# Optimization experiments

Hardware: AMD Instinct MI355X
Metric: run time of the kernel (lower is better)

## Reference

```python
import jax, jax.numpy as jnp
import numpy as np

B, T = 4096, 512
H_ENC, H_DEC = 4, 10


def _cell(x_t, h, c, Wih, Whh, b):
    # PyTorch LSTM cell, gate order i, f, g, o
    g = x_t @ Wih.T + h @ Whh.T + b
    i, f, gg, o = jnp.split(g, 4, axis=-1)
    c = jax.nn.sigmoid(f) * c + jax.nn.sigmoid(i) * jnp.tanh(gg)
    h = jax.nn.sigmoid(o) * jnp.tanh(c)
    return h, c


def _lstm_layer(x_seq, Wih, Whh, bih, bhh):
    # x_seq: [B, T, in] -> outputs [B, T, H], final (h, c) [B, H]
    b = bih + bhh
    Bn = x_seq.shape[0]
    H = Whh.shape[1]
    init = (jnp.zeros((Bn, H), x_seq.dtype), jnp.zeros((Bn, H), x_seq.dtype))

    def step(carry, xt):
        h, c = carry
        h, c = _cell(xt, h, c, Wih, Whh, b)
        return (h, c), h

    (hT, cT), ys = jax.lax.scan(step, init, jnp.swapaxes(x_seq, 0, 1))
    return jnp.swapaxes(ys, 0, 1), hT, cT


def setup_inputs() -> dict:
    key = jax.random.key(0)
    ks = iter(jax.random.split(key, 32))
    p = lambda *s: jax.random.normal(next(ks), s, dtype=jnp.float32) * 0.1
    return {
        "x": jax.random.normal(next(ks), (B, T, 1), dtype=jnp.float32),
        "context": jax.random.normal(next(ks), (B, 1), dtype=jnp.float32),
        "enc_Wih0": p(4 * H_ENC, 1), "enc_Whh0": p(4 * H_ENC, H_ENC),
        "enc_bih0": p(4 * H_ENC), "enc_bhh0": p(4 * H_ENC),
        "enc_Wih1": p(4 * H_ENC, H_ENC), "enc_Whh1": p(4 * H_ENC, H_ENC),
        "enc_bih1": p(4 * H_ENC), "enc_bhh1": p(4 * H_ENC),
        "dec_Wih0": p(4 * H_DEC, 1), "dec_Whh0": p(4 * H_DEC, H_DEC),
        "dec_bih0": p(4 * H_DEC), "dec_bhh0": p(4 * H_DEC),
        "dec_Wih1": p(4 * H_DEC, H_DEC), "dec_Whh1": p(4 * H_DEC, H_DEC),
        "dec_bih1": p(4 * H_DEC), "dec_bhh1": p(4 * H_DEC),
        "fc_W": p(2, H_ENC), "fc_b": p(2),
        "out_W": p(1, H_DEC), "out_b": p(1),
    }


def reference(x, context, enc_Wih0, enc_Whh0, enc_bih0, enc_bhh0,
              enc_Wih1, enc_Whh1, enc_bih1, enc_bhh1,
              dec_Wih0, dec_Whh0, dec_bih0, dec_bhh0,
              dec_Wih1, dec_Whh1, dec_bih1, dec_bhh1,
              fc_W, fc_b, out_W, out_b):
    # ---- encoder: 2-layer LSTM over x [B, T, 1] ----
    y0, h0, c0 = _lstm_layer(x, enc_Wih0, enc_Whh0, enc_bih0, enc_bhh0)
    y1, h1, c1 = _lstm_layer(y0, enc_Wih1, enc_Whh1, enc_bih1, enc_bhh1)
    fwd_out = h1 @ fc_W.T + fc_b  # [B, 2]

    pad = lambda a: jnp.pad(a, ((0, 0), (0, H_DEC - H_ENC)))  # 4 -> 10 units
    b0 = dec_bih0 + dec_bhh0
    b1 = dec_bih1 + dec_bhh1

    def dstep(carry, _):
        hd0, cd0, hd1, cd1 = carry
        inp = hd1[:, :1]  # scalar feedback from top-layer hidden state [B, 1]
        hd0, cd0 = _cell(inp, hd0, cd0, dec_Wih0, dec_Whh0, b0)
        hd1, cd1 = _cell(hd0, hd1, cd1, dec_Wih1, dec_Whh1, b1)
        return (hd0, cd0, hd1, cd1), hd1

    init = (pad(h0), pad(c0), pad(h1), pad(c1))
    _, ys = jax.lax.scan(dstep, init, None, length=x.shape[1])  # [T, B, H_DEC]
    dec_out = jnp.swapaxes(ys, 0, 1)  # [B, T, H_DEC]

    noise = dec_out @ out_W.T + out_b          # [B, T, 1]
    final = noise + fwd_out[:, None, :]        # broadcast -> [B, T, 2]
    return final, fwd_out, noise
```

## Files before the change

kernel.cpp:

```cpp
#include <hip/hip_runtime.h>

#define B_N 4096
#define T_N 512
#define FWD_OFF   (B_N * T_N * 2)
#define NOISE_OFF (FWD_OFF + B_N * 2)

#define S_SIG  (-1.4426950408889634f)
#define S_TANH (-2.8853900817779268f)

typedef float v2f __attribute__((ext_vector_type(2)));
__device__ __forceinline__ v2f mkv2(float a, float b) { v2f r; r.x = a; r.y = b; return r; }

__device__ __forceinline__ v2f pk_fma(v2f a, v2f b, v2f c) {
    v2f d;
    asm("v_pk_fma_f32 %0, %1, %2, %3" : "=v"(d) : "v"(a), "v"(b), "v"(c));
    return d;
}

__device__ __forceinline__ float act_ab(float a, float A, float Bc) {
    float r = __builtin_amdgcn_rcpf(1.0f + __builtin_amdgcn_exp2f(a));
    return fmaf(A, r, Bc);
}
__device__ __forceinline__ float sig_acc(float a) {
    return __builtin_amdgcn_rcpf(1.0f + __builtin_amdgcn_exp2f(a));
}
__device__ __forceinline__ float tanh_acc(float a) {
    return fmaf(2.0f, __builtin_amdgcn_rcpf(1.0f + __builtin_amdgcn_exp2f(a)), -1.0f);
}
__device__ __forceinline__ float tanh_nat(float v) {
    return tanh_acc(v * S_TANH);
}

template<int CTRL>
__device__ __forceinline__ float dppf(float v) {
    return __int_as_float(__builtin_amdgcn_update_dpp(
        __float_as_int(v), __float_as_int(v), CTRL, 0xF, 0xF, false));
}

__global__ __attribute__((amdgpu_waves_per_eu(1, 1))) __launch_bounds__(256)
void fused_kernel(
    const float* __restrict__ x,
    const float* __restrict__ eWih0, const float* __restrict__ eWhh0,
    const float* __restrict__ ebih0, const float* __restrict__ ebhh0,
    const float* __restrict__ eWih1, const float* __restrict__ eWhh1,
    const float* __restrict__ ebih1, const float* __restrict__ ebhh1,
    const float* __restrict__ dWih0, const float* __restrict__ dWhh0,
    const float* __restrict__ dbih0, const float* __restrict__ dbhh0,
    const float* __restrict__ dWih1, const float* __restrict__ dWhh1,
    const float* __restrict__ dbih1, const float* __restrict__ dbhh1,
    const float* __restrict__ fcW, const float* __restrict__ fcb,
    const float* __restrict__ outW, const float* __restrict__ outb,
    float* __restrict__ out)
{
    const int tid  = blockIdx.x * 256 + threadIdx.x;
    const int b    = tid >> 4;
    const int lane = tid & 15;

    const int kk = lane >> 2;
    const float sc = (kk == 2) ? S_TANH : S_SIG;
    const float Ak = (kk == 2) ? 2.0f : 1.0f;
    const float Bk = (kk == 2) ? -1.0f : 0.0f;

    v2f h0p[2] = {mkv2(0.f, 0.f), mkv2(0.f, 0.f)};
    v2f h1p[2] = {mkv2(0.f, 0.f), mkv2(0.f, 0.f)};
    float c0 = 0.f, c1 = 0.f;
    float fw0, fw1;

    {
        const int r = lane;
        float ew0 = eWih0[r] * sc;
        float eb0 = (ebih0[r] + ebhh0[r]) * sc;
        float eb1 = (ebih1[r] + ebhh1[r]) * sc;
        v2f ewh0p[2], ewi1p[2], ewh1p[2];
#pragma unroll
        for (int j = 0; j < 2; ++j) {
            ewh0p[j] = mkv2(eWhh0[r * 4 + 2 * j], eWhh0[r * 4 + 2 * j + 1]) * sc;
            ewi1p[j] = mkv2(eWih1[r * 4 + 2 * j], eWih1[r * 4 + 2 * j + 1]) * sc;
            ewh1p[j] = mkv2(eWhh1[r * 4 + 2 * j], eWhh1[r * 4 + 2 * j + 1]) * sc;
        }

        const float4* __restrict__ xq4 = (const float4*)(x + (long)b * T_N);
        float4 xq = xq4[0];

        auto estep = [&](float xc) {
            v2f pp = pk_fma(ewh1p[0], h1p[0], mkv2(eb1, 0.f));
            pp = pk_fma(ewh1p[1], h1p[1], pp);

            v2f gg = pk_fma(ewh0p[0], h0p[0], mkv2(fmaf(ew0, xc, eb0), 0.f));
            gg = pk_fma(ewh0p[1], h0p[1], gg);
            float gate = act_ab(gg.x + gg.y, Ak, Bk);
            float fv = dppf<0x12C>(gate);
            float gv = dppf<0x128>(gate);
            float ov = dppf<0x124>(gate);
            c0 = fmaf(fv, c0, gate * gv);
            float h0u = ov * tanh_nat(c0);
            h0p[0].x = dppf<0x150>(h0u); h0p[0].y = dppf<0x151>(h0u);
            h0p[1].x = dppf<0x152>(h0u); h0p[1].y = dppf<0x153>(h0u);

            v2f qq = pk_fma(ewi1p[0], h0p[0], pp);
            qq = pk_fma(ewi1p[1], h0p[1], qq);
            float gate1 = act_ab(qq.x + qq.y, Ak, Bk);
            fv = dppf<0x12C>(gate1);
            gv = dppf<0x128>(gate1);
            ov = dppf<0x124>(gate1);
            c1 = fmaf(fv, c1, gate1 * gv);
            float h1u = ov * tanh_nat(c1);
            h1p[0].x = dppf<0x150>(h1u); h1p[0].y = dppf<0x151>(h1u);
            h1p[1].x = dppf<0x152>(h1u); h1p[1].y = dppf<0x153>(h1u);
        };

        for (int tb = 0; tb < T_N / 4; ++tb) {
            float4 xn = (tb + 1 < T_N / 4) ? xq4[tb + 1] : xq;
            estep(xq.x); estep(xq.y); estep(xq.z); estep(xq.w);
            xq = xn;
        }

        fw0 = fcb[0];
        fw1 = fcb[1];
        fw0 = fmaf(fcW[0], h1p[0].x, fw0); fw0 = fmaf(fcW[1], h1p[0].y, fw0);
        fw0 = fmaf(fcW[2], h1p[1].x, fw0); fw0 = fmaf(fcW[3], h1p[1].y, fw0);
        fw1 = fmaf(fcW[4], h1p[0].x, fw1); fw1 = fmaf(fcW[5], h1p[0].y, fw1);
        fw1 = fmaf(fcW[6], h1p[1].x, fw1); fw1 = fmaf(fcW[7], h1p[1].y, fw1);
        if (lane == 0) {
            out[FWD_OFF + b * 2 + 0] = fw0;
            out[FWD_OFF + b * 2 + 1] = fw1;
        }
    }

    const int uc = (lane < 10) ? lane : 9;

    float wih0r[4], b0r[4], b1r[4];
    v2f whh0p[4][5], wih1p[4][5], whh1p[4][5];
#pragma unroll
    for (int k = 0; k < 4; ++k) {
        const int r = k * 10 + uc;
        const float sck = (k == 2) ? S_TANH : S_SIG;
        wih0r[k] = dWih0[r] * sck;
        b0r[k] = (dbih0[r] + dbhh0[r]) * sck;
        b1r[k] = (dbih1[r] + dbhh1[r]) * sck;
#pragma unroll
        for (int j = 0; j < 5; ++j) {
            whh0p[k][j] = mkv2(dWhh0[r * 10 + 2 * j], dWhh0[r * 10 + 2 * j + 1]) * sck;
            wih1p[k][j] = mkv2(dWih1[r * 10 + 2 * j], dWih1[r * 10 + 2 * j + 1]) * sck;
            whh1p[k][j] = mkv2(dWhh1[r * 10 + 2 * j], dWhh1[r * 10 + 2 * j + 1]) * sck;
        }
    }
    v2f outwp[5];
#pragma unroll
    for (int j = 0; j < 5; ++j) outwp[j] = mkv2(outW[2 * j], outW[2 * j + 1]);
    const float outb0 = outb[0];

    v2f dh0p[5], dh1p[5];
    dh0p[0] = h0p[0]; dh0p[1] = h0p[1];
    dh1p[0] = h1p[0]; dh1p[1] = h1p[1];
#pragma unroll
    for (int j = 2; j < 5; ++j) { dh0p[j] = mkv2(0.f, 0.f); dh1p[j] = mkv2(0.f, 0.f); }
    float dc0 = (lane < 4) ? c0 : 0.f;
    float dc1 = (lane < 4) ? c1 : 0.f;

    float my_noise = 0.f;

    for (int t = 0; t < T_N; ++t) {
        const float inp = dh1p[0].x;

        v2f p1[4];
#pragma unroll
        for (int k = 0; k < 4; ++k) {
            p1[k] = pk_fma(whh1p[k][0], dh1p[0], mkv2(b1r[k], 0.f));
#pragma unroll
            for (int j = 1; j < 5; ++j) p1[k] = pk_fma(whh1p[k][j], dh1p[j], p1[k]);
        }

        v2f g2[4];
#pragma unroll
        for (int k = 0; k < 4; ++k) {
            g2[k] = pk_fma(whh0p[k][0], dh0p[0], mkv2(fmaf(wih0r[k], inp, b0r[k]), 0.f));
#pragma unroll
            for (int j = 1; j < 5; ++j) g2[k] = pk_fma(whh0p[k][j], dh0p[j], g2[k]);
        }
        float iv = sig_acc(g2[0].x + g2[0].y);
        float fv = sig_acc(g2[1].x + g2[1].y);
        float gv = tanh_acc(g2[2].x + g2[2].y);
        float ov = sig_acc(g2[3].x + g2[3].y);
        dc0 = fmaf(fv, dc0, iv * gv);
        const float h0u = ov * tanh_nat(dc0);
        dh0p[0].x = dppf<0x150>(h0u); dh0p[0].y = dppf<0x151>(h0u);
        dh0p[1].x = dppf<0x152>(h0u); dh0p[1].y = dppf<0x153>(h0u);
        dh0p[2].x = dppf<0x154>(h0u); dh0p[2].y = dppf<0x155>(h0u);
        dh0p[3].x = dppf<0x156>(h0u); dh0p[3].y = dppf<0x157>(h0u);
        dh0p[4].x = dppf<0x158>(h0u); dh0p[4].y = dppf<0x159>(h0u);

#pragma unroll
        for (int k = 0; k < 4; ++k) {
#pragma unroll
            for (int j = 0; j < 5; ++j) p1[k] = pk_fma(wih1p[k][j], dh0p[j], p1[k]);
        }
        iv = sig_acc(p1[0].x + p1[0].y);
        fv = sig_acc(p1[1].x + p1[1].y);
        gv = tanh_acc(p1[2].x + p1[2].y);
        ov = sig_acc(p1[3].x + p1[3].y);
        dc1 = fmaf(fv, dc1, iv * gv);
        const float h1u = ov * tanh_nat(dc1);
        dh1p[0].x = dppf<0x150>(h1u); dh1p[0].y = dppf<0x151>(h1u);
        dh1p[1].x = dppf<0x152>(h1u); dh1p[1].y = dppf<0x153>(h1u);
        dh1p[2].x = dppf<0x154>(h1u); dh1p[2].y = dppf<0x155>(h1u);
        dh1p[3].x = dppf<0x156>(h1u); dh1p[3].y = dppf<0x157>(h1u);
        dh1p[4].x = dppf<0x158>(h1u); dh1p[4].y = dppf<0x159>(h1u);

        v2f na = pk_fma(outwp[0], dh1p[0], mkv2(outb0, 0.f));
#pragma unroll
        for (int j = 1; j < 5; ++j) na = pk_fma(outwp[j], dh1p[j], na);
        const float nz = na.x + na.y;

        my_noise = ((t & 15) == lane) ? nz : my_noise;
        if ((t & 15) == 15) {
            const int idx = b * T_N + (t - 15) + lane;
            out[NOISE_OFF + idx] = my_noise;
            float2 fin;
            fin.x = my_noise + fw0;
            fin.y = my_noise + fw1;
            ((float2*)out)[idx] = fin;
        }
    }
}

extern "C" void kernel_launch(void* const* d_in, const int* in_sizes, int n_in,
                              void* d_out, int out_size, void* d_ws, size_t ws_size,
                              hipStream_t stream) {
    const float* x     = (const float*)d_in[0];
    const float* eWih0 = (const float*)d_in[2];
    const float* eWhh0 = (const float*)d_in[3];
    const float* ebih0 = (const float*)d_in[4];
    const float* ebhh0 = (const float*)d_in[5];
    const float* eWih1 = (const float*)d_in[6];
    const float* eWhh1 = (const float*)d_in[7];
    const float* ebih1 = (const float*)d_in[8];
    const float* ebhh1 = (const float*)d_in[9];
    const float* dWih0 = (const float*)d_in[10];
    const float* dWhh0 = (const float*)d_in[11];
    const float* dbih0 = (const float*)d_in[12];
    const float* dbhh0 = (const float*)d_in[13];
    const float* dWih1 = (const float*)d_in[14];
    const float* dWhh1 = (const float*)d_in[15];
    const float* dbih1 = (const float*)d_in[16];
    const float* dbhh1 = (const float*)d_in[17];
    const float* fcW   = (const float*)d_in[18];
    const float* fcb   = (const float*)d_in[19];
    const float* outW  = (const float*)d_in[20];
    const float* outb  = (const float*)d_in[21];

    float* out = (float*)d_out;

    fused_kernel<<<dim3((B_N * 16) / 256), dim3(256), 0, stream>>>(
        x, eWih0, eWhh0, ebih0, ebhh0, eWih1, eWhh1, ebih1, ebhh1,
        dWih0, dWhh0, dbih0, dbhh0, dWih1, dWhh1, dbih1, dbhh1,
        fcW, fcb, outW, outb, out);
}
```

Before: 365.4 us.

## Skew LSTM layers across timesteps and move bias adds off the critical path

The encoder loop is software-pipelined so that layer 1's dot products for step t-1 are computed alongside layer 0's for step t. A prologue and epilogue handle the first and last steps. In the decoder, the output projection and store for step t-1 move ahead of the current step's activations, and bias and input terms are added after the packed dot products rather than seeding them. This is meant to shorten the serial dependency chain per timestep and give more independent work to hide latency, at the cost of extra code complexity and a separate final store block.

```diff
diff --git a/kernel.cpp b/kernel.cpp
--- a/kernel.cpp
+++ b/kernel.cpp
@@ -14,6 +14,11 @@
 __device__ __forceinline__ v2f pk_fma(v2f a, v2f b, v2f c) {
     v2f d;
     asm("v_pk_fma_f32 %0, %1, %2, %3" : "=v"(d) : "v"(a), "v"(b), "v"(c));
+    return d;
+}
+__device__ __forceinline__ v2f pk_mul(v2f a, v2f b) {
+    v2f d;
+    asm("v_pk_mul_f32 %0, %1, %2" : "=v"(d) : "v"(a), "v"(b));
     return d;
 }
 
@@ -79,41 +84,49 @@
             ewh1p[j] = mkv2(eWhh1[r * 4 + 2 * j], eWhh1[r * 4 + 2 * j + 1]) * sc;
         }
 
-        const float4* __restrict__ xq4 = (const float4*)(x + (long)b * T_N);
-        float4 xq = xq4[0];
-
-        auto estep = [&](float xc) {
-            v2f pp = pk_fma(ewh1p[0], h1p[0], mkv2(eb1, 0.f));
-            pp = pk_fma(ewh1p[1], h1p[1], pp);
-
-            v2f gg = pk_fma(ewh0p[0], h0p[0], mkv2(fmaf(ew0, xc, eb0), 0.f));
+        auto l0_dots = [&](float xc) -> float {
+            v2f gg = pk_mul(ewh0p[0], h0p[0]);
             gg = pk_fma(ewh0p[1], h0p[1], gg);
-            float gate = act_ab(gg.x + gg.y, Ak, Bk);
+            return gg.x + gg.y + fmaf(ew0, xc, eb0);
+        };
+        auto l1_dots = [&]() -> float {
+            v2f qq = pk_mul(ewi1p[0], h0p[0]);
+            qq = pk_fma(ewi1p[1], h0p[1], qq);
+            qq = pk_fma(ewh1p[0], h1p[0], qq);
+            qq = pk_fma(ewh1p[1], h1p[1], qq);
+            return qq.x + qq.y + eb1;
+        };
+        auto finish = [&](float g, float& c, v2f* hp) {
+            float gate = act_ab(g, Ak, Bk);
             float fv = dppf<0x12C>(gate);
             float gv = dppf<0x128>(gate);
             float ov = dppf<0x124>(gate);
-            c0 = fmaf(fv, c0, gate * gv);
-            float h0u = ov * tanh_nat(c0);
-            h0p[0].x = dppf<0x150>(h0u); h0p[0].y = dppf<0x151>(h0u);
-            h0p[1].x = dppf<0x152>(h0u); h0p[1].y = dppf<0x153>(h0u);
-
-            v2f qq = pk_fma(ewi1p[0], h0p[0], pp);
-            qq = pk_fma(ewi1p[1], h0p[1], qq);
-            float gate1 = act_ab(qq.x + qq.y, Ak, Bk);
-            fv = dppf<0x12C>(gate1);
-            gv = dppf<0x128>(gate1);
-            ov = dppf<0x124>(gate1);
-            c1 = fmaf(fv, c1, gate1 * gv);
-            float h1u = ov * tanh_nat(c1);
-            h1p[0].x = dppf<0x150>(h1u); h1p[0].y = dppf<0x151>(h1u);
-            h1p[1].x = dppf<0x152>(h1u); h1p[1].y = dppf<0x153>(h1u);
-        };
-
-        for (int tb = 0; tb < T_N / 4; ++tb) {
-            float4 xn = (tb + 1 < T_N / 4) ? xq4[tb + 1] : xq;
-            estep(xq.x); estep(xq.y); estep(xq.z); estep(xq.w);
+            c = fmaf(fv, c, gate * gv);
+            float hu = ov * tanh_nat(c);
+            hp[0].x = dppf<0x150>(hu); hp[0].y = dppf<0x151>(hu);
+            hp[1].x = dppf<0x152>(hu); hp[1].y = dppf<0x153>(hu);
+        };
+        auto ebody = [&](float xc) {
+            float g1 = l1_dots();
+            float g0 = l0_dots(xc);
+            finish(g0, c0, h0p);
+            finish(g1, c1, h1p);
+        };
+
+        const float4* __restrict__ xq4 = (const float4*)(x + (long)b * T_N);
+        float4 xq = xq4[0];
+        float4 xn = xq4[1];
+
+        { float g0 = l0_dots(xq.x); finish(g0, c0, h0p); }
+        ebody(xq.y); ebody(xq.z); ebody(xq.w);
+        xq = xn;
+#pragma unroll 1
+        for (int tb = 1; tb < T_N / 4; ++tb) {
+            xn = (tb + 1 < T_N / 4) ? xq4[tb + 1] : xq;
+            ebody(xq.x); ebody(xq.y); ebody(xq.z); ebody(xq.w);
             xq = xn;
         }
+        { float g1 = l1_dots(); finish(g1, c1, h1p); }
 
         fw0 = fcb[0];
         fw1 = fcb[1];
@@ -166,7 +179,7 @@
         v2f p1[4];
 #pragma unroll
         for (int k = 0; k < 4; ++k) {
-            p1[k] = pk_fma(whh1p[k][0], dh1p[0], mkv2(b1r[k], 0.f));
+            p1[k] = pk_mul(whh1p[k][0], dh1p[0]);
 #pragma unroll
             for (int j = 1; j < 5; ++j) p1[k] = pk_fma(whh1p[k][j], dh1p[j], p1[k]);
         }
@@ -174,14 +187,31 @@
         v2f g2[4];
 #pragma unroll
         for (int k = 0; k < 4; ++k) {
-            g2[k] = pk_fma(whh0p[k][0], dh0p[0], mkv2(fmaf(wih0r[k], inp, b0r[k]), 0.f));
+            g2[k] = pk_mul(whh0p[k][0], dh0p[0]);
 #pragma unroll
             for (int j = 1; j < 5; ++j) g2[k] = pk_fma(whh0p[k][j], dh0p[j], g2[k]);
         }
-        float iv = sig_acc(g2[0].x + g2[0].y);
-        float fv = sig_acc(g2[1].x + g2[1].y);
-        float gv = tanh_acc(g2[2].x + g2[2].y);
-        float ov = sig_acc(g2[3].x + g2[3].y);
+
+        {
+            v2f na = pk_mul(outwp[0], dh1p[0]);
+#pragma unroll
+            for (int j = 1; j < 5; ++j) na = pk_fma(outwp[j], dh1p[j], na);
+            const float nzp = na.x + na.y + outb0;
+            my_noise = (((t - 1) & 15) == lane) ? nzp : my_noise;
+        }
+        if ((t & 15) == 0 && t) {
+            const int idx = b * T_N + (t - 16) + lane;
+            out[NOISE_OFF + idx] = my_noise;
+            float2 fin;
+            fin.x = my_noise + fw0;
+            fin.y = my_noise + fw1;
+            ((float2*)out)[idx] = fin;
+        }
+
+        float iv = sig_acc(g2[0].x + g2[0].y + fmaf(wih0r[0], inp, b0r[0]));
+        float fv = sig_acc(g2[1].x + g2[1].y + fmaf(wih0r[1], inp, b0r[1]));
+        float gv = tanh_acc(g2[2].x + g2[2].y + fmaf(wih0r[2], inp, b0r[2]));
+        float ov = sig_acc(g2[3].x + g2[3].y + fmaf(wih0r[3], inp, b0r[3]));
         dc0 = fmaf(fv, dc0, iv * gv);
         const float h0u = ov * tanh_nat(dc0);
         dh0p[0].x = dppf<0x150>(h0u); dh0p[0].y = dppf<0x151>(h0u);
@@ -195,10 +225,10 @@
 #pragma unroll
             for (int j = 0; j < 5; ++j) p1[k] = pk_fma(wih1p[k][j], dh0p[j], p1[k]);
         }
-        iv = sig_acc(p1[0].x + p1[0].y);
-        fv = sig_acc(p1[1].x + p1[1].y);
-        gv = tanh_acc(p1[2].x + p1[2].y);
-        ov = sig_acc(p1[3].x + p1[3].y);
+        iv = sig_acc(p1[0].x + p1[0].y + b1r[0]);
+        fv = sig_acc(p1[1].x + p1[1].y + b1r[1]);
+        gv = tanh_acc(p1[2].x + p1[2].y + b1r[2]);
+        ov = sig_acc(p1[3].x + p1[3].y + b1r[3]);
         dc1 = fmaf(fv, dc1, iv * gv);
         const float h1u = ov * tanh_nat(dc1);
         dh1p[0].x = dppf<0x150>(h1u); dh1p[0].y = dppf<0x151>(h1u);
@@ -206,21 +236,20 @@
         dh1p[2].x = dppf<0x154>(h1u); dh1p[2].y = dppf<0x155>(h1u);
         dh1p[3].x = dppf<0x156>(h1u); dh1p[3].y = dppf<0x157>(h1u);
         dh1p[4].x = dppf<0x158>(h1u); dh1p[4].y = dppf<0x159>(h1u);
-
-        v2f na = pk_fma(outwp[0], dh1p[0], mkv2(outb0, 0.f));
+    }
+
+    {
+        v2f na = pk_mul(outwp[0], dh1p[0]);
 #pragma unroll
         for (int j = 1; j < 5; ++j) na = pk_fma(outwp[j], dh1p[j], na);
-        const float nz = na.x + na.y;
-
-        my_noise = ((t & 15) == lane) ? nz : my_noise;
-        if ((t & 15) == 15) {
-            const int idx = b * T_N + (t - 15) + lane;
-            out[NOISE_OFF + idx] = my_noise;
-            float2 fin;
-            fin.x = my_noise + fw0;
-            fin.y = my_noise + fw1;
-            ((float2*)out)[idx] = fin;
-        }
+        const float nz = na.x + na.y + outb0;
+        my_noise = (lane == 15) ? nz : my_noise;
+        const int idx = b * T_N + (T_N - 16) + lane;
+        out[NOISE_OFF + idx] = my_noise;
+        float2 fin;
+        fin.x = my_noise + fw0;
+        fin.y = my_noise + fw1;
+        ((float2*)out)[idx] = fin;
     }
 }
 
```

Result: slower. 378.5 us (+3.6%).
